# Optimization experiments

Measured on AMD Instinct MI355X. Metric: run time of the kernel, lower is better.

The kernel has to match this reference:

```python
import jax, jax.numpy as jnp
import numpy as np

NQ = 10          # qubits
NT = 32          # tokens (LCU terms)
DM = 512         # d_model
DEG = 2          # qsvt degree
B = 128          # batch
NPQC = 4 * NQ    # params per PQC application
DIM = 2 ** NQ    # statevector dimension


def ansatz14_spec(q, layers=1):
    spec = []
    for _ in range(layers):
        spec += [('ry', (i,)) for i in range(q)]
        spec += [('crx', (i, (i + 1) % q)) for i in range(q - 1, -1, -1)]
        spec += [('ry', (i,)) for i in range(q)]
        spec += [('crx', (i, (i - 1) % q)) for i in [q - 1] + list(range(q - 1))]
    return spec

SPEC = ansatz14_spec(NQ, 1)


def _gate_ry(theta):
    h = theta * 0.5
    c = jnp.cos(h)
    s = jnp.sin(h)
    m = jnp.stack([jnp.stack([c, -s], -1), jnp.stack([s, c], -1)], -2)
    return m.astype(jnp.complex64)  # (N,2,2)


def _gate_rx(theta):
    h = theta * 0.5
    c = jnp.cos(h).astype(jnp.complex64)
    s = (-1j) * jnp.sin(h).astype(jnp.complex64)
    return jnp.stack([jnp.stack([c, s], -1), jnp.stack([s, c], -1)], -2)


def _apply_1q(state, mats, wire, q):
    # state: (N, 2^q) complex; mats: (N,2,2); wire 0 is most significant bit
    N = state.shape[0]
    a = 2 ** wire
    bdim = 2 ** (q - wire - 1)
    s = state.reshape(N, a, 2, bdim)
    return jnp.einsum('nij,najb->naib', mats, s).reshape(N, 2 ** q)


def _apply_crx(state, theta, c, t, q):
    # controlled-RX: control wire c, target wire t
    N = state.shape[0]
    st = state.reshape((N,) + (2,) * q)
    ax = 1 + c
    s0 = jnp.take(st, 0, axis=ax)   # control = 0 branch: untouched
    s1 = jnp.take(st, 1, axis=ax)   # control = 1 branch: apply RX on target
    tp = t if t < c else t - 1      # target wire position after removing control axis
    s1n = _apply_1q(s1.reshape(N, -1), _gate_rx(theta), tp, q - 1).reshape(s1.shape)
    return jnp.stack([s0, s1n], axis=ax).reshape(N, 2 ** q)


def _apply_pqc(state, params, q):
    # params: (N, NPQC); fixed small gate list -> Python loop is fine
    for k, (fn, w) in enumerate(SPEC):
        th = params[:, k]
        if fn == 'ry':
            state = _apply_1q(state, _gate_ry(th), w[0], q)
        else:
            state = _apply_crx(state, th, w[0], w[1], q)
    return state


def _apply_lcu(states, params, lcu):
    # states: (B, DIM) complex; params: (B, L, NPQC); lcu: (B, L) complex
    Bn, L = lcu.shape
    rep = jnp.repeat(states, L, axis=0)                    # (B*L, DIM)
    st = _apply_pqc(rep, params.reshape(Bn * L, NPQC), NQ)
    return jnp.einsum('bld,bl->bd', st.reshape(Bn, L, DIM), lcu)


def _measure_xyz(state, q):
    # Pauli expectations per wire: order [X_0..X_{q-1}, Y_0.., Z_0..]
    N = state.shape[0]
    xs, ys, zs = [], [], []
    for w in range(q):
        s = state.reshape(N, 2 ** w, 2, -1)
        a0, a1 = s[:, :, 0, :], s[:, :, 1, :]
        cross = jnp.sum(jnp.conj(a0) * a1, axis=(1, 2))
        xs.append(2.0 * jnp.real(cross))
        ys.append(2.0 * jnp.imag(cross))
        zs.append(jnp.sum(jnp.abs(a0) ** 2 - jnp.abs(a1) ** 2, axis=(1, 2)))
    return jnp.stack(xs + ys + zs, axis=1).astype(jnp.float32)  # (B, 3q)


def reference(tokens_emb, W, b, lcu_re, lcu_im, qsvt_coeffs, ff_params):
    Bn, L, D = tokens_emb.shape
    L = min(L, NT)
    pqc_params = tokens_emb[:, :L] @ W.T + b               # (B, L, NPQC)
    lcu = (lcu_re + 1j * lcu_im).astype(jnp.complex64)[:L]
    lcu = lcu / jnp.sum(jnp.abs(lcu))
    lcu_b = jnp.broadcast_to(lcu[None], (Bn, L))
    init = jnp.zeros((Bn, DIM), jnp.complex64).at[:, 0].set(1.0)
    acc = qsvt_coeffs[0].astype(jnp.complex64) * init
    mono = init
    for k in range(1, DEG + 1):
        mono = _apply_lcu(mono, pqc_params, lcu_b)
        acc = acc + qsvt_coeffs[k].astype(jnp.complex64) * mono
    state = acc / jnp.sum(jnp.abs(qsvt_coeffs))
    state = state / jnp.linalg.norm(state, axis=-1, keepdims=True)
    ffp = jnp.broadcast_to(ff_params[None], (Bn, NPQC))
    state = _apply_pqc(state, ffp, NQ)
    return _measure_xyz(state, NQ)


def setup_inputs():
    key = jax.random.key(0)
    ks = jax.random.split(key, 7)
    return {
        'tokens_emb': jax.random.normal(ks[0], (B, NT, DM), jnp.float32),
        'W': jax.random.normal(ks[1], (NPQC, DM), jnp.float32) * 0.05,
        'b': jax.random.normal(ks[2], (NPQC,), jnp.float32),
        'lcu_re': jax.random.normal(ks[3], (NT,), jnp.float32),
        'lcu_im': jax.random.normal(ks[4], (NT,), jnp.float32),
        'qsvt_coeffs': jax.random.normal(ks[5], (DEG + 1,), jnp.float32),
        'ff_params': jax.random.normal(ks[6], (NPQC,), jnp.float32),
    }
```

## Files before the change

### kernel.cpp

```cpp
#include <hip/hip_runtime.h>
#include <hip/hip_bf16.h>


#define NQ   10
#define NT   32
#define DM   512
#define BATCH 128
#define NPQC 40
#define DIM  1024
#define PSTRIDE (BATCH * DIM)

typedef float v2f __attribute__((ext_vector_type(2)));

#define WAITLDS asm volatile("s_waitcnt lgkmcnt(0)" ::: "memory")

__device__ __forceinline__ v2f Jrot(v2f v) {
  return __builtin_shufflevector(v, -v, 1, 2);
}
__device__ __forceinline__ v2f Jc(v2f v) {
  return __builtin_shufflevector(-v, v, 1, 2);
}


template<int B>
__device__ __forceinline__ void g_ry(v2f (&a)[16], float c, float s) {
  static_assert(B >= 6, "RY targets must be register bits");
  constexpr int m = 1 << (B - 6);
#pragma unroll
  for (int r = 0; r < 16; ++r) {
    if (!(r & m)) {
      int r1 = r | m;
      v2f a0 = a[r], a1 = a[r1];
      a[r]  = c * a0 - s * a1;
      a[r1] = s * a0 + c * a1;
    }
  }
}

template<int BC, int BT>
__device__ __forceinline__ void g_crx(v2f (&a)[16], int lane, float c, float s) {
  static_assert(BT >= 6, "CRX targets must be register bits");
  constexpr int m = 1 << (BT - 6);
  bool lane_ok = (BC >= 6) || ((lane >> BC) & 1);
  float ce = lane_ok ? c : 1.f;
  float se = lane_ok ? s : 0.f;
#pragma unroll
  for (int r = 0; r < 16; ++r) {
    if (!(r & m)) {
      if constexpr (BC >= 6) { if (!((r >> (BC - 6)) & 1)) continue; }
      int r1 = r | m;
      v2f a0 = a[r], a1 = a[r1];
      a[r]  = ce * a0 + se * Jrot(a1);
      a[r1] = ce * a1 + se * Jrot(a0);
    }
  }
}

template<int L0, int L1, int L2, int L3>
__device__ __forceinline__ void remap(v2f (&a)[16], v2f* __restrict__ slab,
                                      int lane) {
  constexpr int LM = (1 << L0) | (1 << L1) | (1 << L2) | (1 << L3);
#pragma unroll
  for (int r = 0; r < 16; ++r) {
    int f = 0;
    if (L0 < 4 && (r & 1)) f |= 1 << L0;
    if (L1 < 4 && (r & 2)) f |= 1 << L1;
    if (L2 < 4 && (r & 4)) f |= 1 << L2;
    if (L3 < 4 && (r & 8)) f |= 1 << L3;
    slab[r * 64 + (lane ^ f)] = a[r];
  }
  WAITLDS;
  int la = lane & ~LM & 63;
  la |= ((lane >> L0) & 1) << 6;
  la |= ((lane >> L1) & 1) << 7;
  la |= ((lane >> L2) & 1) << 8;
  la |= ((lane >> L3) & 1) << 9;
  if (L0 < 4) la |= ((lane >> L0) & 1) << L0;
  if (L1 < 4) la |= ((lane >> L1) & 1) << L1;
  if (L2 < 4) la |= ((lane >> L2) & 1) << L2;
  if (L3 < 4) la |= ((lane >> L3) & 1) << L3;
#pragma unroll
  for (int r = 0; r < 16; ++r) {
    int rc = ((r & 1) ? (1 << L0) : 0) | ((r & 2) ? (1 << L1) : 0)
           | ((r & 4) ? (1 << L2) : 0) | ((r & 8) ? (1 << L3) : 0);
    a[r] = slab[la ^ rc];
  }
}

template<bool SKIP_HEAD>
__device__ __forceinline__ void apply_pqc_phased(v2f (&a)[16],
    const float2* __restrict__ cs, v2f* __restrict__ slab, int lane) {
#define RYt(B, t)      g_ry<B>(a, t.x, t.y);
#define CXt(BC, BT, t) g_crx<BC, BT>(a, lane, t.x, t.y);
  float2 t10 = cs[10], t11 = cs[11], t12 = cs[12];
  if constexpr (!SKIP_HEAD) {
    float2 t0 = cs[0], t1 = cs[1], t2 = cs[2], t3 = cs[3];
    float2 t4 = cs[4], t5 = cs[5], t6 = cs[6], t7 = cs[7];
    float2 t8 = cs[8], t9 = cs[9];
    RYt(9,t0) RYt(8,t1) RYt(7,t2) RYt(6,t3)
    remap<5,4,3,2>(a, slab, lane);
    RYt(6,t4) RYt(7,t5) RYt(8,t6) RYt(9,t7)
    remap<1,0,2,3>(a, slab, lane);
    RYt(6,t8) RYt(7,t9)
  }
  CXt(7,8,t10) CXt(6,7,t11) CXt(3,6,t12)
  float2 t13 = cs[13], t14 = cs[14], t15 = cs[15], t16 = cs[16];
  remap<1,0,2,3>(a, slab, lane);
  CXt(8,9,t13) CXt(7,8,t14) CXt(6,7,t15) CXt(5,6,t16)
  float2 t17 = cs[17], t18 = cs[18], t19 = cs[19];
  float2 t20 = cs[20], t21 = cs[21], t22 = cs[22], t23 = cs[23];
  remap<2,3,4,5>(a, slab, lane);
  CXt(8,9,t17) CXt(7,8,t18) CXt(6,7,t19)
  RYt(6,t20) RYt(7,t21) RYt(8,t22) RYt(9,t23)
  float2 t24 = cs[24], t25 = cs[25], t26 = cs[26], t27 = cs[27];
  remap<2,3,4,5>(a, slab, lane);
  RYt(6,t24) RYt(7,t25) RYt(8,t26) RYt(9,t27)
  float2 t28 = cs[28], t29 = cs[29];
  float2 t30 = cs[30], t31 = cs[31], t32 = cs[32], t33 = cs[33];
  remap<1,0,2,3>(a, slab, lane);
  RYt(6,t28) RYt(7,t29)
  CXt(7,6,t30) CXt(8,7,t31) CXt(9,8,t32) CXt(4,9,t33)
  float2 t34 = cs[34], t35 = cs[35], t36 = cs[36], t37 = cs[37];
  remap<4,5,1,0>(a, slab, lane);
  CXt(7,6,t34) CXt(8,7,t35) CXt(9,8,t36) CXt(2,9,t37)
  float2 t38 = cs[38], t39 = cs[39];
  remap<2,3,4,5>(a, slab, lane);
  CXt(7,6,t38) CXt(8,7,t39)
#undef RYt
#undef CXt
}

__device__ __forceinline__ int p8_lane_canon(int lane) {
  return (((lane >> 1) & 1) << 9) | ((lane & 1) << 8) | (((lane >> 2) & 1) << 7)
       | (((lane >> 3) & 1) << 6) | (((lane >> 4) & 1) << 5) | (((lane >> 5) & 1) << 4);
}

__device__ __forceinline__ void stagger(int key) {
  int s = key & 3;
  if (s & 1) __builtin_amdgcn_s_sleep(1);
  if (s & 2) __builtin_amdgcn_s_sleep(2);
}

__global__ __launch_bounds__(256) void params_kernel(
    const float* __restrict__ emb, const float* __restrict__ W,
    const float* __restrict__ bias,
    const float* __restrict__ lcu_re, const float* __restrict__ lcu_im,
    const float* __restrict__ ffp,
    float2* __restrict__ cs, float2* __restrict__ ffcs, float2* __restrict__ lcu) {
  int blk = blockIdx.x;
  int tid = threadIdx.x;
  if (blk == 256) {
    if (tid < NPQC) {
      float h = 0.5f * ffp[tid];
      ffcs[tid] = make_float2(cosf(h), sinf(h));
    }
    if (tid == 64) {
      float ssum = 0.f;
      for (int i = 0; i < NT; ++i) {
        float re = lcu_re[i], im = lcu_im[i];
        ssum += sqrtf(re * re + im * im);
      }
      float inv = 1.f / ssum;
      for (int i = 0; i < NT; ++i)
        lcu[i] = make_float2(lcu_re[i] * inv, lcu_im[i] * inv);
    }
    return;
  }

  __shared__ float Asl[16 * 516];
  int row0 = blk * 16;

  const float4* eg = (const float4*)(emb + (size_t)row0 * DM);
#pragma unroll
  for (int i = 0; i < 8; ++i) {
    int e = tid + i * 256;
    int r = e >> 7, k4 = e & 127;
    float4 v = eg[e];
    *(float4*)&Asl[r * 516 + k4 * 4] = v;
  }
  __syncthreads();

  int kq = tid >> 6;
  int lane = tid & 63;
  int rg = lane >> 3;
  int cg = lane & 7;

  const float* Ar0 = &Asl[(2 * rg) * 516 + kq * 128];
  const float* Ar1 = Ar0 + 516;
  const float* Bg  = W + (size_t)(5 * cg) * DM + kq * 128;

  float acc[2][5] = {};
#pragma unroll 4
  for (int k = 0; k < 128; k += 4) {
    float4 a0 = *(const float4*)(Ar0 + k);
    float4 a1 = *(const float4*)(Ar1 + k);
#pragma unroll
    for (int j = 0; j < 5; ++j) {
      float4 b = *(const float4*)(Bg + j * DM + k);
      acc[0][j] += a0.x * b.x + a0.y * b.y + a0.z * b.z + a0.w * b.w;
      acc[1][j] += a1.x * b.x + a1.y * b.y + a1.z * b.z + a1.w * b.w;
    }
  }

  __syncthreads();
  float* red = Asl;
#pragma unroll
  for (int i = 0; i < 2; ++i)
#pragma unroll
    for (int j = 0; j < 5; ++j)
      red[kq * 644 + (2 * rg + i) * 40 + 5 * cg + j] = acc[i][j];
  __syncthreads();

  for (int o = tid; o < 640; o += 256) {
    float v = bias[o % 40] + red[o] + red[644 + o] + red[1288 + o] + red[1932 + o];
    float h = 0.5f * v;
    cs[(size_t)blk * 640 + o] = make_float2(cosf(h), sinf(h));
  }
}

template<bool FIRST>
__global__ __launch_bounds__(256) void pqc_step(
    const float2* __restrict__ cs, const float2* __restrict__ lcu,
    const v2f* __restrict__ src, v2f* __restrict__ dst) {
  __shared__ v2f slabs[4][1024];
  int lane = threadIdx.x & 63;
  int wvu = __builtin_amdgcn_readfirstlane(threadIdx.x >> 6);
  int blk = blockIdx.x;
  stagger(blk + wvu);
  int b = blk >> 3, qq = blk & 7;
  int l = qq * 4 + wvu;
  const float2* csrow = cs + (size_t)(b * NT + l) * NPQC;
  v2f* slab = slabs[wvu];

  v2f a[16];
  if constexpr (FIRST) {
    float2 f5 = csrow[5], f4 = csrow[4], f6 = csrow[6], f7 = csrow[7];
    float2 f2 = csrow[2], f3 = csrow[3];
    float2 f8 = csrow[8], f9 = csrow[9], f0 = csrow[0], f1 = csrow[1];
    float lp = ((lane & 1) ? f5.y : f5.x);
    lp *= ((lane & 2) ? f4.y : f4.x);
    lp *= ((lane & 4) ? f6.y : f6.x);
    lp *= ((lane & 8) ? f7.y : f7.x);
    lp *= ((lane & 16) ? f2.y : f2.x);
    lp *= ((lane & 32) ? f3.y : f3.x);
#pragma unroll
    for (int r = 0; r < 16; ++r) {
      float rp = ((r & 1) ? f8.y : f8.x) * ((r & 2) ? f9.y : f9.x)
               * ((r & 4) ? f0.y : f0.x) * ((r & 8) ? f1.y : f1.x);
      a[r].x = lp * rp;
      a[r].y = 0.f;
    }
  } else {
    const v2f* s = src + (size_t)b * DIM;
#pragma unroll
    for (int r = 0; r < 16; ++r) a[r] = s[r * 64 + lane];
  }

  apply_pqc_phased<FIRST>(a, csrow, slab, lane);

  float2 w = lcu[l];
  int pl = p8_lane_canon(lane);
  pl ^= (pl >> 5);
#pragma unroll
  for (int r = 0; r < 16; ++r) {
    int rc = ((r & 1) << 3) | ((r & 2) << 1) | ((r & 4) >> 1) | ((r & 8) >> 3);
    slab[pl ^ rc] = w.x * a[r] + w.y * Jc(a[r]);
  }
  __syncthreads();

  v2f* dst_b = dst + (size_t)(qq * BATCH + b) * DIM;
#pragma unroll
  for (int i = 0; i < 4; ++i) {
    int n = threadIdx.x + i * 256;
    int ph = n ^ (n >> 5);
    v2f sum = slabs[0][ph] + slabs[1][ph] + slabs[2][ph] + slabs[3][ph];
    dst_b[n] = sum;
  }
}


__global__ __launch_bounds__(256) void reduce_slices(v2f* __restrict__ buf) {
  int n = blockIdx.x * 256 + threadIdx.x;
  v2f acc = buf[n];
#pragma unroll
  for (int q = 1; q < 8; ++q) acc += buf[n + q * PSTRIDE];
  buf[n] = acc;
}

__global__ __launch_bounds__(256) void final_fused(
    const v2f* __restrict__ red1, const v2f* __restrict__ part2,
    const float* __restrict__ qsvt, const float2* __restrict__ ffcs,
    float* __restrict__ out) {
  __shared__ v2f st[1024];
  __shared__ float2 ang[40];
  __shared__ float rbuf[4];
  __shared__ float tb[30 * 257];
  int b = blockIdx.x, tid = threadIdx.x;
  int lane = tid & 63, wv = tid >> 6;
  float q0 = qsvt[0], q1 = qsvt[1], q2 = qsvt[2];
  const v2f* r1 = red1 + (size_t)b * DIM;
  const v2f* p2 = part2 + (size_t)b * DIM;

  if (tid < NPQC) ang[tid] = ffcs[tid];

  v2f vals[4];
  float nn = 0.f;
#pragma unroll
  for (int i = 0; i < 4; ++i) {
    int n = tid + i * 256;
    v2f m2 = p2[n];
#pragma unroll
    for (int q = 1; q < 8; ++q) m2 += p2[n + q * PSTRIDE];
    v2f v = q1 * r1[n] + q2 * m2;
    if (n == 0) v.x += q0;
    vals[i] = v;
    nn += v.x * v.x + v.y * v.y;
  }
#pragma unroll
  for (int o = 1; o < 64; o <<= 1) nn += __shfl_xor(nn, o);
  if (lane == 0) rbuf[wv] = nn;
  __syncthreads();
  float inv = 1.f / sqrtf(rbuf[0] + rbuf[1] + rbuf[2] + rbuf[3]);
#pragma unroll
  for (int i = 0; i < 4; ++i) {
    int n = tid + i * 256;
    st[n ^ (n >> 5)] = vals[i] * inv;
  }
  __syncthreads();

#pragma unroll 1
  for (int k = 0; k < NPQC; ++k) {
    int isCrx, c, t;
    if (k < 10)      { isCrx = 0; t = k;      c = 0; }
    else if (k < 20) { int i = 19 - k; isCrx = 1; c = i; t = (i == 9) ? 0 : i + 1; }
    else if (k < 30) { isCrx = 0; t = k - 20; c = 0; }
    else             { int i = (k == 30) ? 9 : k - 31; isCrx = 1; c = i; t = (i == 0) ? 9 : i - 1; }
    int m  = 1 << (9 - t);
    int cb = 9 - c;
    float2 th = ang[k];
    float cg = th.x, sg = th.y;

    v2f a0[2], a1[2];
    int j0[2], j1[2], en[2];
#pragma unroll
    for (int p = 0; p < 2; ++p) {
      int qp = p * 256 + tid;
      int i0 = ((qp & ~(m - 1)) << 1) | (qp & (m - 1));
      int i1 = i0 | m;
      j0[p] = i0 ^ (i0 >> 5);
      j1[p] = i1 ^ (i1 >> 5);
      en[p] = (i0 >> cb) & 1;
      a0[p] = st[j0[p]];
      a1[p] = st[j1[p]];
    }
#pragma unroll
    for (int p = 0; p < 2; ++p) {
      v2f n0, n1;
      if (!isCrx) {
        n0 = cg * a0[p] - sg * a1[p];
        n1 = sg * a0[p] + cg * a1[p];
      } else {
        float ce = en[p] ? cg : 1.f;
        float se = en[p] ? sg : 0.f;
        n0 = ce * a0[p] + se * Jrot(a1[p]);
        n1 = ce * a1[p] + se * Jrot(a0[p]);
      }
      st[j0[p]] = n0;
      st[j1[p]] = n1;
    }
    __syncthreads();
  }

#pragma unroll 1
  for (int w = 0; w < NQ; ++w) {
    int m = 1 << (9 - w);
    float xr = 0.f, xi = 0.f, zz = 0.f;
#pragma unroll
    for (int p = 0; p < 2; ++p) {
      int qp = p * 256 + tid;
      int i0 = ((qp & ~(m - 1)) << 1) | (qp & (m - 1));
      int i1 = i0 | m;
      v2f a0 = st[i0 ^ (i0 >> 5)];
      v2f a1 = st[i1 ^ (i1 >> 5)];
      xr += a0.x * a1.x + a0.y * a1.y;
      xi += a0.x * a1.y - a0.y * a1.x;
      zz += a0.x * a0.x + a0.y * a0.y - a1.x * a1.x - a1.y * a1.y;
    }
    tb[w * 257 + tid]        = xr;
    tb[(10 + w) * 257 + tid] = xi;
    tb[(20 + w) * 257 + tid] = zz;
  }
  __syncthreads();
  if (tid < 30) {
    float s2 = 0.f;
#pragma unroll 8
    for (int t = 0; t < 256; ++t) s2 += tb[tid * 257 + t];
    float sc = (tid < 20) ? 2.f : 1.f;
    out[b * 30 + tid] = sc * s2;
  }
}


extern "C" void kernel_launch(void* const* d_in, const int* in_sizes, int n_in,
                              void* d_out, int out_size, void* d_ws, size_t ws_size,
                              hipStream_t stream) {
  const float* emb    = (const float*)d_in[0];
  const float* W      = (const float*)d_in[1];
  const float* bias   = (const float*)d_in[2];
  const float* lcu_re = (const float*)d_in[3];
  const float* lcu_im = (const float*)d_in[4];
  const float* qsvt   = (const float*)d_in[5];
  const float* ffp    = (const float*)d_in[6];
  float* out = (float*)d_out;

  char* ws = (char*)d_ws;
  float2* cs    = (float2*)ws;
  float2* ffcs  = (float2*)(ws + 1310720);
  float2* lcu   = (float2*)(ws + 1311040);
  v2f*    part1 = (v2f*)(ws + 1311744);
  v2f*    part2 = (v2f*)(ws + 1311744 + 8388608);

  params_kernel<<<257, 256, 0, stream>>>(emb, W, bias, lcu_re, lcu_im, ffp,
                                         cs, ffcs, lcu);
  pqc_step<true><<<1024, 256, 0, stream>>>(cs, lcu, nullptr, part1);
  reduce_slices<<<512, 256, 0, stream>>>(part1);
  pqc_step<false><<<1024, 256, 0, stream>>>(cs, lcu, part1, part2);
  final_fused<<<BATCH, 256, 0, stream>>>(part1, part2, qsvt, ffcs, out);
}
```

Before: 151.4 us.

## Replace slice buffers and reduce kernel with atomic accumulation into zeroed outputs

Each pqc_step block now atomically adds its four-term partial sum straight into a single per-batch output buffer instead of writing one of eight slices. That removes the reduce_slices launch and the eight-way slice reads in the final kernel. The params kernel gets extra blocks that zero both accumulation buffers. The final kernel also switches its measurement reduction from a big LDS table to wave shuffles. The cost is eight-way float atomic contention per element and non-deterministic summation order.

Measured after the change: 148.3 us (median of 2 runs). 1.02x faster.

```diff
diff --git a/kernel.cpp b/kernel.cpp
--- a/kernel.cpp
+++ b/kernel.cpp
@@ -8,7 +8,7 @@
 #define BATCH 128
 #define NPQC 40
 #define DIM  1024
-#define PSTRIDE (BATCH * DIM)
+#define SLICE_V2F (BATCH * DIM)
 
 typedef float v2f __attribute__((ext_vector_type(2)));
 
@@ -146,9 +146,17 @@
     const float* __restrict__ bias,
     const float* __restrict__ lcu_re, const float* __restrict__ lcu_im,
     const float* __restrict__ ffp,
-    float2* __restrict__ cs, float2* __restrict__ ffcs, float2* __restrict__ lcu) {
+    float2* __restrict__ cs, float2* __restrict__ ffcs, float2* __restrict__ lcu,
+    v2f* __restrict__ part1, v2f* __restrict__ part2) {
   int blk = blockIdx.x;
   int tid = threadIdx.x;
+  if (blk >= 257) {
+    int idx = (blk - 257) * 256 + tid;
+    v2f z = (v2f)(0.f);
+    if (idx < SLICE_V2F) part1[idx] = z;
+    else                 part2[idx - SLICE_V2F] = z;
+    return;
+  }
   if (blk == 256) {
     if (tid < NPQC) {
       float h = 0.5f * ffp[tid];
@@ -223,8 +231,9 @@
     const float2* __restrict__ cs, const float2* __restrict__ lcu,
     const v2f* __restrict__ src, v2f* __restrict__ dst) {
   __shared__ v2f slabs[4][1024];
-  int lane = threadIdx.x & 63;
-  int wvu = __builtin_amdgcn_readfirstlane(threadIdx.x >> 6);
+  int tid = threadIdx.x;
+  int lane = tid & 63;
+  int wvu = __builtin_amdgcn_readfirstlane(tid >> 6);
   int blk = blockIdx.x;
   stagger(blk + wvu);
   int b = blk >> 3, qq = blk & 7;
@@ -268,38 +277,30 @@
   }
   __syncthreads();
 
-  v2f* dst_b = dst + (size_t)(qq * BATCH + b) * DIM;
+  float* df = (float*)(dst + (size_t)b * DIM);
 #pragma unroll
   for (int i = 0; i < 4; ++i) {
-    int n = threadIdx.x + i * 256;
+    int n = tid + i * 256;
     int ph = n ^ (n >> 5);
     v2f sum = slabs[0][ph] + slabs[1][ph] + slabs[2][ph] + slabs[3][ph];
-    dst_b[n] = sum;
-  }
-}
-
-
-__global__ __launch_bounds__(256) void reduce_slices(v2f* __restrict__ buf) {
-  int n = blockIdx.x * 256 + threadIdx.x;
-  v2f acc = buf[n];
-#pragma unroll
-  for (int q = 1; q < 8; ++q) acc += buf[n + q * PSTRIDE];
-  buf[n] = acc;
+    atomicAdd(df + 2 * n,     sum.x);
+    atomicAdd(df + 2 * n + 1, sum.y);
+  }
 }
 
 __global__ __launch_bounds__(256) void final_fused(
-    const v2f* __restrict__ red1, const v2f* __restrict__ part2,
+    const v2f* __restrict__ red1, const v2f* __restrict__ red2b,
     const float* __restrict__ qsvt, const float2* __restrict__ ffcs,
     float* __restrict__ out) {
   __shared__ v2f st[1024];
   __shared__ float2 ang[40];
   __shared__ float rbuf[4];
-  __shared__ float tb[30 * 257];
+  __shared__ float red2[120];
   int b = blockIdx.x, tid = threadIdx.x;
-  int lane = tid & 63, wv = tid >> 6;
+  int lane = tid & 63, wvu = tid >> 6;
   float q0 = qsvt[0], q1 = qsvt[1], q2 = qsvt[2];
   const v2f* r1 = red1 + (size_t)b * DIM;
-  const v2f* p2 = part2 + (size_t)b * DIM;
+  const v2f* p2 = red2b + (size_t)b * DIM;
 
   if (tid < NPQC) ang[tid] = ffcs[tid];
 
@@ -308,17 +309,14 @@
 #pragma unroll
   for (int i = 0; i < 4; ++i) {
     int n = tid + i * 256;
-    v2f m2 = p2[n];
-#pragma unroll
-    for (int q = 1; q < 8; ++q) m2 += p2[n + q * PSTRIDE];
-    v2f v = q1 * r1[n] + q2 * m2;
+    v2f v = q1 * r1[n] + q2 * p2[n];
     if (n == 0) v.x += q0;
     vals[i] = v;
     nn += v.x * v.x + v.y * v.y;
   }
 #pragma unroll
   for (int o = 1; o < 64; o <<= 1) nn += __shfl_xor(nn, o);
-  if (lane == 0) rbuf[wv] = nn;
+  if (lane == 0) rbuf[wvu] = nn;
   __syncthreads();
   float inv = 1.f / sqrtf(rbuf[0] + rbuf[1] + rbuf[2] + rbuf[3]);
 #pragma unroll
@@ -371,7 +369,8 @@
     __syncthreads();
   }
 
-#pragma unroll 1
+  float prt[30];
+#pragma unroll
   for (int w = 0; w < NQ; ++w) {
     int m = 1 << (9 - w);
     float xr = 0.f, xi = 0.f, zz = 0.f;
@@ -386,15 +385,22 @@
       xi += a0.x * a1.y - a0.y * a1.x;
       zz += a0.x * a0.x + a0.y * a0.y - a1.x * a1.x - a1.y * a1.y;
     }
-    tb[w * 257 + tid]        = xr;
-    tb[(10 + w) * 257 + tid] = xi;
-    tb[(20 + w) * 257 + tid] = zz;
+    prt[w]      = xr;
+    prt[10 + w] = xi;
+    prt[20 + w] = zz;
+  }
+#pragma unroll
+  for (int v = 0; v < 30; ++v) {
+#pragma unroll
+    for (int o = 1; o < 64; o <<= 1) prt[v] += __shfl_xor(prt[v], o);
+  }
+  if (lane == 0) {
+#pragma unroll
+    for (int v = 0; v < 30; ++v) red2[wvu * 30 + v] = prt[v];
   }
   __syncthreads();
   if (tid < 30) {
-    float s2 = 0.f;
-#pragma unroll 8
-    for (int t = 0; t < 256; ++t) s2 += tb[tid * 257 + t];
+    float s2 = red2[tid] + red2[30 + tid] + red2[60 + tid] + red2[90 + tid];
     float sc = (tid < 20) ? 2.f : 1.f;
     out[b * 30 + tid] = sc * s2;
   }
@@ -418,12 +424,11 @@
   float2* ffcs  = (float2*)(ws + 1310720);
   float2* lcu   = (float2*)(ws + 1311040);
   v2f*    part1 = (v2f*)(ws + 1311744);
-  v2f*    part2 = (v2f*)(ws + 1311744 + 8388608);
-
-  params_kernel<<<257, 256, 0, stream>>>(emb, W, bias, lcu_re, lcu_im, ffp,
-                                         cs, ffcs, lcu);
+  v2f*    part2 = (v2f*)(ws + 1311744 + 1048576);
+
+  params_kernel<<<1281, 256, 0, stream>>>(emb, W, bias, lcu_re, lcu_im, ffp,
+                                          cs, ffcs, lcu, part1, part2);
   pqc_step<true><<<1024, 256, 0, stream>>>(cs, lcu, nullptr, part1);
-  reduce_slices<<<512, 256, 0, stream>>>(part1);
   pqc_step<false><<<1024, 256, 0, stream>>>(cs, lcu, part1, part2);
   final_fused<<<BATCH, 256, 0, stream>>>(part1, part2, qsvt, ffcs, out);
 }
```
